# Performance work log

Hardware: AMD Instinct MI355X
Metric: run time of the kernel (lower is better)

Reference implementation:

```python
import jax, jax.numpy as jnp
import numpy as np

B, S, D = 4, 2048, 1024
H = 16
DH = D // H


def setup_inputs() -> dict:
    key = jax.random.key(0)
    ks = jax.random.split(key, 5)
    scale = 1.0 / np.sqrt(D)
    return {
        "x": jax.random.normal(ks[0], (B, S, D), dtype=jnp.float32),
        "wq": jax.random.normal(ks[1], (D, D), dtype=jnp.float32) * scale,
        "wk": jax.random.normal(ks[2], (D, D), dtype=jnp.float32) * scale,
        "wv": jax.random.normal(ks[3], (D, D), dtype=jnp.float32) * scale,
        "wo": jax.random.normal(ks[4], (D, D), dtype=jnp.float32) * scale,
    }


def reference(x, wq, wk, wv, wo):
    b, s, d = x.shape
    # nn.Linear applies x @ W.T (weights are [out, in])
    q = (x @ wq.T).reshape(b, s, H, DH).transpose(0, 2, 1, 3)  # [b,h,s,dh]
    k = (x @ wk.T).reshape(b, s, H, DH).transpose(0, 2, 1, 3)
    v = (x @ wv.T).reshape(b, s, H, DH).transpose(0, 2, 1, 3)
    scale = 1.0 / jnp.sqrt(jnp.asarray(DH, dtype=x.dtype))
    scores = jnp.einsum("bhqd,bhkd->bhqk", q, k) * scale  # [b,h,s,s]
    causal = jnp.tril(jnp.ones((s, s), dtype=bool))
    scores = jnp.where(causal, scores, -jnp.inf)
    attn = jax.nn.softmax(scores, axis=-1)
    out = jnp.einsum("bhqk,bhkd->bhqd", attn, v)  # [b,h,s,dh]
    out = out.transpose(0, 2, 1, 3).reshape(b, s, d)
    return out @ wo.T
```

## Files before the change

kernel.cpp:

```cpp
#include <hip/hip_runtime.h>
#include <hip/hip_bf16.h>

#define Bz 4
#define Sz 2048
#define Dz 1024
#define Hz 16
#define DHz 64

typedef __bf16 bf16x8 __attribute__((ext_vector_type(8)));
typedef float f32x4 __attribute__((ext_vector_type(4)));
typedef short s16x4 __attribute__((ext_vector_type(4)));
typedef unsigned short u16x4 __attribute__((ext_vector_type(4)));

__global__ __launch_bounds__(256) void cvt_f32_bf16(const float* __restrict__ src,
                                                    __hip_bfloat16* __restrict__ dst, int n) {
    int i = (blockIdx.x * 256 + threadIdx.x) * 4;
    if (i >= n) return;
    float4 f = *reinterpret_cast<const float4*>(src + i);
    dst[i + 0] = __float2bfloat16(f.x);
    dst[i + 1] = __float2bfloat16(f.y);
    dst[i + 2] = __float2bfloat16(f.z);
    dst[i + 3] = __float2bfloat16(f.w);
}

__global__ __launch_bounds__(256) void cvt_w4(const float* __restrict__ w0, const float* __restrict__ w1,
                                              const float* __restrict__ w2, const float* __restrict__ w3,
                                              __hip_bfloat16* __restrict__ dst) {
    constexpr int WEL = Dz * Dz;
    int i = (blockIdx.x * 256 + threadIdx.x) * 4;
    const int which = i >> 20;
    const float* src = (which == 0) ? w0 : (which == 1) ? w1 : (which == 2) ? w2 : w3;
    float4 f = *reinterpret_cast<const float4*>(src + (i & (WEL - 1)));
    dst[i + 0] = __float2bfloat16(f.x);
    dst[i + 1] = __float2bfloat16(f.y);
    dst[i + 2] = __float2bfloat16(f.z);
    dst[i + 3] = __float2bfloat16(f.w);
}

__device__ __forceinline__ void gl2lds16(const __hip_bfloat16* g, __hip_bfloat16* l) {
    __builtin_amdgcn_global_load_lds(
        (const __attribute__((address_space(1))) void*)g,
        (__attribute__((address_space(3))) void*)l, 16, 0, 0);
}

__device__ __forceinline__ unsigned ldsaddr(const void* p) {
    return (unsigned)(size_t)(const __attribute__((address_space(3))) void*)p;
}

template <int N, int K, typename OT, int MODE>
__device__ __forceinline__ void gemm128_body(const __hip_bfloat16* __restrict__ A,
                                             const __hip_bfloat16* __restrict__ W,
                                             OT* __restrict__ C, int bm, int bn,
                                             __hip_bfloat16* As, __hip_bfloat16* Bs) {
    const int tid  = threadIdx.x;
    const int wid  = tid >> 6;
    const int lane = tid & 63;
    const int quad = lane >> 4;
    const int l16  = lane & 15;
    const int wr = wid >> 1, wc = wid & 1;

    const int srow = wid * 32 + (lane >> 2);
    const int scol = (lane & 3) * 8;
    const __hip_bfloat16* gA = A + (size_t)(bm * 128 + srow) * K + scol;
    const __hip_bfloat16* gB = W + (size_t)(bn * 128 + srow) * K + scol;
    __hip_bfloat16* lA = &As[(wid * 32) * 32];
    __hip_bfloat16* lB = &Bs[(wid * 32) * 32];

    f32x4 acc[4][4] = {};

    for (int k0 = 0; k0 < K; k0 += 32) {
        __syncthreads();
        gl2lds16(gA + k0,                  lA);
        gl2lds16(gA + (size_t)16 * K + k0, lA + 16 * 32);
        gl2lds16(gB + k0,                  lB);
        gl2lds16(gB + (size_t)16 * K + k0, lB + 16 * 32);
        __syncthreads();

        bf16x8 af[4], bf[4];
#pragma unroll
        for (int mi = 0; mi < 4; ++mi)
            af[mi] = *reinterpret_cast<const bf16x8*>(&As[(wr * 64 + mi * 16 + l16) * 32 + quad * 8]);
#pragma unroll
        for (int ni = 0; ni < 4; ++ni)
            bf[ni] = *reinterpret_cast<const bf16x8*>(&Bs[(wc * 64 + ni * 16 + l16) * 32 + quad * 8]);
#pragma unroll
        for (int mi = 0; mi < 4; ++mi)
#pragma unroll
            for (int ni = 0; ni < 4; ++ni)
                acc[mi][ni] = __builtin_amdgcn_mfma_f32_16x16x32_bf16(af[mi], bf[ni], acc[mi][ni], 0, 0, 0);
    }

#pragma unroll
    for (int mi = 0; mi < 4; ++mi)
#pragma unroll
        for (int ni = 0; ni < 4; ++ni) {
            const int row0 = bm * 128 + wr * 64 + mi * 16 + quad * 4;
            const int col  = bn * 128 + wc * 64 + ni * 16 + l16;
#pragma unroll
            for (int r = 0; r < 4; ++r) {
                const int row = row0 + r;
                if constexpr (MODE == 0) {
                    if constexpr (__is_same(OT, float))
                        C[(size_t)row * N + col] = acc[mi][ni][r];
                    else
                        C[(size_t)row * N + col] = __float2bfloat16(acc[mi][ni][r]);
                } else if constexpr (MODE == 1) {
                    const int bh = (row >> 11) * Hz + (col >> 6);
                    C[(size_t)bh * (Sz * DHz) + (size_t)(row & 2047) * 64 + (col & 63)] =
                        __float2bfloat16(acc[mi][ni][r]);
                } else {
                    const int bh = (row >> 11) * Hz + (col >> 6);
                    C[(size_t)bh * (Sz * DHz) + (size_t)((col >> 4) & 3) * (Sz * 16) +
                      (size_t)(row & 2047) * 16 + (col & 15)] = __float2bfloat16(acc[mi][ni][r]);
                }
            }
        }
}

template <int M, int N, int K, typename OT>
__global__ __launch_bounds__(256) void gemm128(const __hip_bfloat16* __restrict__ A,
                                               const __hip_bfloat16* __restrict__ W,
                                               OT* __restrict__ C) {
    __shared__ __hip_bfloat16 As[128 * 32];
    __shared__ __hip_bfloat16 Bs[128 * 32];
    constexpr int NB = N / 128;
    gemm128_body<N, K, OT, 0>(A, W, C, blockIdx.x / NB, blockIdx.x % NB, As, Bs);
}

template <int M, int K>
__global__ __launch_bounds__(256) void gemm_qkv(const __hip_bfloat16* __restrict__ A,
                                                const __hip_bfloat16* __restrict__ W0,
                                                const __hip_bfloat16* __restrict__ W1,
                                                const __hip_bfloat16* __restrict__ W2,
                                                __hip_bfloat16* __restrict__ C0,
                                                __hip_bfloat16* __restrict__ C1,
                                                __hip_bfloat16* __restrict__ C2) {
    __shared__ __hip_bfloat16 As[128 * 32];
    __shared__ __hip_bfloat16 Bs[128 * 32];
    constexpr int NB = Dz / 128;
    const int which = blockIdx.x % 3;
    const int rem   = blockIdx.x / 3;
    const int bm = rem / NB, bn = rem % NB;
    if (which == 0)      gemm128_body<Dz, K, __hip_bfloat16, 0>(A, W0, C0, bm, bn, As, Bs);
    else if (which == 1) gemm128_body<Dz, K, __hip_bfloat16, 1>(A, W1, C1, bm, bn, As, Bs);
    else                 gemm128_body<Dz, K, __hip_bfloat16, 2>(A, W2, C2, bm, bn, As, Bs);
}

__device__ __forceinline__ f32x4 mfma16bf(s16x4 a, s16x4 b, f32x4 c) {
#if __has_builtin(__builtin_amdgcn_mfma_f32_16x16x16bf16_1k)
    return __builtin_amdgcn_mfma_f32_16x16x16bf16_1k(a, b, c, 0, 0, 0);
#else
    asm volatile("v_mfma_f32_16x16x16_bf16 %0, %1, %2, %0" : "+v"(c) : "v"(a), "v"(b));
    return c;
#endif
}

#define TRD(i, off) \
    asm volatile("ds_read_b64_tr_b16 %0, %1 offset:" off : "=v"(vf[i]) : "v"(va))

__global__ __launch_bounds__(256, 4) void attn_mfma6(const __hip_bfloat16* __restrict__ Q,
                                                     const __hip_bfloat16* __restrict__ Kh,
                                                     const __hip_bfloat16* __restrict__ Vh,
                                                     __hip_bfloat16* __restrict__ O) {
    __shared__ __hip_bfloat16 Ks[2][64 * 64];
    __shared__ __hip_bfloat16 Vs[2][64 * 64];

    const int tid  = threadIdx.x;
    const int wid  = tid >> 6;
    const int lane = tid & 63;
    const int quad = lane >> 4;
    const int l16  = lane & 15;

    const int xcd  = blockIdx.x & 7;
    const int j    = blockIdx.x >> 3;
    const int bh   = xcd * 8 + (j >> 4);
    const int pair = j & 15;
    const int h    = bh & 15;
    const int b    = bh >> 4;
    const size_t baseQ = (size_t)b * Sz * Dz + (size_t)h * DHz;
    const size_t kvb   = (size_t)bh * (Sz * DHz);

    const int rlo = lane >> 3;
    const int xel = ((lane & 7) ^ rlo) * 8;

    auto stage = [&](int kn, int bf_) {
#pragma unroll
        for (int c = 0; c < 2; ++c) {
            gl2lds16(Kh + kvb + (size_t)(kn + wid * 16 + c * 8 + rlo) * 64 + xel,
                     &Ks[bf_][(wid * 16 + c * 8) * 64]);
            gl2lds16(Vh + kvb + (size_t)wid * (Sz * 16) + (size_t)(kn + c * 32 + (lane >> 1)) * 16 + (lane & 1) * 8,
                     &Vs[bf_][wid * 1024 + c * 512]);
        }
    };

    const unsigned vb0 = ldsaddr(&Vs[0][0]) + lane * 8;
    const unsigned sw  = (l16 & 7) << 4;

    constexpr float SC = 0.18033688011112042f;

    int buf = 0;
    stage(0, 0);
    __syncthreads();

#pragma unroll 1
    for (int p = 0; p < 2; ++p) {
        const int qblk  = (p == 0) ? pair : 31 - pair;
        const int q0    = qblk * 64 + wid * 16;
        const int niter = qblk + 1;

        const __hip_bfloat16* qp = Q + baseQ + (size_t)(q0 + l16) * Dz + quad * 8;
        const bf16x8 qf0 = *reinterpret_cast<const bf16x8*>(qp);
        const bf16x8 qf1 = *reinterpret_cast<const bf16x8*>(qp + 32);

        float m = -1e30f, l = 0.f;
        f32x4 ot[4] = {};

#pragma unroll 1
        for (int it = 0; it < niter; ++it) {
            const int k0 = it * 64;

            f32x4 st[4] = {};
            {
                const char* Kp = (const char*)&Ks[buf][0];
#pragma unroll
                for (int s = 0; s < 4; ++s) {
                    const int rb = (s * 16 + l16) * 128;
                    const bf16x8 a0 = *reinterpret_cast<const bf16x8*>(Kp + rb + ((quad * 16) ^ sw));
                    const bf16x8 a1 = *reinterpret_cast<const bf16x8*>(Kp + rb + ((quad * 16 + 64) ^ sw));
                    st[s] = __builtin_amdgcn_mfma_f32_16x16x32_bf16(a0, qf0, st[s], 0, 0, 0);
                    st[s] = __builtin_amdgcn_mfma_f32_16x16x32_bf16(a1, qf1, st[s], 0, 0, 0);
                }
            }

            const bool more = (it + 1 < niter);
            if (more)        stage(k0 + 64, buf ^ 1);
            else if (p == 0) stage(0,       buf ^ 1);

            float sv[16];
            if (it == niter - 1) {
                const int qrow = q0 + l16;
#pragma unroll
                for (int s = 0; s < 4; ++s)
#pragma unroll
                    for (int r = 0; r < 4; ++r) {
                        const int key = k0 + s * 16 + quad * 4 + r;
                        sv[s * 4 + r] = (key <= qrow) ? st[s][r] * SC : -1e30f;
                    }
            } else {
#pragma unroll
                for (int s = 0; s < 4; ++s)
#pragma unroll
                    for (int r = 0; r < 4; ++r) sv[s * 4 + r] = st[s][r] * SC;
            }

            float mx[8];
#pragma unroll
            for (int i = 0; i < 8; ++i) mx[i] = fmaxf(sv[2 * i], sv[2 * i + 1]);
#pragma unroll
            for (int i = 0; i < 4; ++i) mx[i] = fmaxf(mx[2 * i], mx[2 * i + 1]);
            float tmax = fmaxf(fmaxf(mx[0], mx[1]), fmaxf(mx[2], mx[3]));
            tmax = fmaxf(tmax, __shfl_xor(tmax, 16, 64));
            tmax = fmaxf(tmax, __shfl_xor(tmax, 32, 64));

            const float mnew = fmaxf(m, tmax);
            const bool  skip = __all(tmax <= m);
            float alpha = 1.f;
            if (!skip) { alpha = __builtin_amdgcn_exp2f(m - mnew); m = mnew; }

            float pv[16];
#pragma unroll
            for (int i = 0; i < 16; ++i) pv[i] = __builtin_amdgcn_exp2f(sv[i] - m);

            float ad[8];
#pragma unroll
            for (int i = 0; i < 8; ++i) ad[i] = pv[2 * i] + pv[2 * i + 1];
#pragma unroll
            for (int i = 0; i < 4; ++i) ad[i] = ad[2 * i] + ad[2 * i + 1];
            float psum = (ad[0] + ad[1]) + (ad[2] + ad[3]);
            psum += __shfl_xor(psum, 16, 64);
            psum += __shfl_xor(psum, 32, 64);
            l = l * alpha + psum;

            s16x4 vf[16];
            const unsigned va = vb0 + (unsigned)(buf << 13);
            TRD(0, "0");    TRD(1, "512");  TRD(2, "1024"); TRD(3, "1536");
            TRD(4, "2048"); TRD(5, "2560"); TRD(6, "3072"); TRD(7, "3584");

            s16x4 pw[4];
#pragma unroll
            for (int s = 0; s < 4; ++s)
#pragma unroll
                for (int r = 0; r < 4; ++r) {
                    union { __hip_bfloat16 hh; short uu; } cv;
                    cv.hh = __float2bfloat16(pv[s * 4 + r]);
                    pw[s][r] = cv.uu;
                }
            if (!skip) {
#pragma unroll
                for (int s = 0; s < 4; ++s) ot[s] *= alpha;
            }

            asm volatile("s_waitcnt lgkmcnt(0)" ::: "memory");
            __builtin_amdgcn_sched_barrier(0);
            TRD(8,  "4096"); TRD(9,  "4608"); TRD(10, "5120"); TRD(11, "5632");
            TRD(12, "6144"); TRD(13, "6656"); TRD(14, "7168"); TRD(15, "7680");

            ot[0] = mfma16bf(vf[0],  pw[0], ot[0]);
            ot[0] = mfma16bf(vf[1],  pw[1], ot[0]);
            ot[0] = mfma16bf(vf[2],  pw[2], ot[0]);
            ot[0] = mfma16bf(vf[3],  pw[3], ot[0]);
            ot[1] = mfma16bf(vf[4],  pw[0], ot[1]);
            ot[1] = mfma16bf(vf[5],  pw[1], ot[1]);
            ot[1] = mfma16bf(vf[6],  pw[2], ot[1]);
            ot[1] = mfma16bf(vf[7],  pw[3], ot[1]);

            asm volatile("s_waitcnt lgkmcnt(0)" ::: "memory");
            __builtin_amdgcn_sched_barrier(0);
            ot[2] = mfma16bf(vf[8],  pw[0], ot[2]);
            ot[2] = mfma16bf(vf[9],  pw[1], ot[2]);
            ot[2] = mfma16bf(vf[10], pw[2], ot[2]);
            ot[2] = mfma16bf(vf[11], pw[3], ot[2]);
            ot[3] = mfma16bf(vf[12], pw[0], ot[3]);
            ot[3] = mfma16bf(vf[13], pw[1], ot[3]);
            ot[3] = mfma16bf(vf[14], pw[2], ot[3]);
            ot[3] = mfma16bf(vf[15], pw[3], ot[3]);

            __syncthreads();
            buf ^= 1;
        }

        const float linv = 1.f / l;
        __hip_bfloat16* op = O + baseQ + (size_t)(q0 + l16) * Dz + quad * 4;
#pragma unroll
        for (int sd = 0; sd < 4; ++sd) {
            u16x4 w;
#pragma unroll
            for (int r = 0; r < 4; ++r) {
                union { __hip_bfloat16 hh; unsigned short uu; } cv;
                cv.hh = __float2bfloat16(ot[sd][r] * linv);
                w[r] = cv.uu;
            }
            *reinterpret_cast<u16x4*>(op + sd * 16) = w;
        }
    }
}

extern "C" void kernel_launch(void* const* d_in, const int* in_sizes, int n_in,
                              void* d_out, int out_size, void* d_ws, size_t ws_size,
                              hipStream_t stream) {
    const float* x  = (const float*)d_in[0];
    const float* wq = (const float*)d_in[1];
    const float* wk = (const float*)d_in[2];
    const float* wv = (const float*)d_in[3];
    const float* wo = (const float*)d_in[4];
    float* out = (float*)d_out;

    constexpr int TOK = Bz * Sz * Dz;
    constexpr int WEL = Dz * Dz;

    __hip_bfloat16* xb  = (__hip_bfloat16*)d_ws;
    __hip_bfloat16* wqb = xb  + TOK;
    __hip_bfloat16* wkb = wqb + WEL;
    __hip_bfloat16* wvb = wkb + WEL;
    __hip_bfloat16* wob = wvb + WEL;
    __hip_bfloat16* Qb  = wob + WEL;
    __hip_bfloat16* Kh  = Qb + TOK;
    __hip_bfloat16* Vh  = (__hip_bfloat16*)d_out;
    __hip_bfloat16* Ob  = xb;

    cvt_f32_bf16<<<TOK / 4 / 256, 256, 0, stream>>>(x, xb, TOK);
    cvt_w4<<<4 * WEL / 4 / 256, 256, 0, stream>>>(wq, wk, wv, wo, wqb);

    constexpr int M = Bz * Sz;
    constexpr int GB = (M / 128) * (Dz / 128);

    gemm_qkv<M, Dz><<<3 * GB, 256, 0, stream>>>(xb, wqb, wkb, wvb, Qb, Kh, Vh);

    const int ATTN_BLOCKS = Bz * Hz * 16;
    attn_mfma6<<<ATTN_BLOCKS, 256, 0, stream>>>(Qb, Kh, Vh, Ob);

    gemm128<M, Dz, Dz, float><<<GB, 256, 0, stream>>>(Ob, wob, out);
}
```

Measured before the change: 249.5 us.

## Fold softmax scale into Q projection and compute row sums with MFMA

Multiplies the softmax scale (with log2e) into Q in the QKV GEMM epilogue, so the attention kernel no longer scales every score. The per-row probability sum is now accumulated by MFMA against a vector of ones instead of a VALU add tree plus cross-lane shuffles. The running max uses a flatter fmax chain, and alpha rescaling moves inside the non-skip branch. This trades VALU and shuffle work for a few extra MFMAs per tile, and rounding Q to bf16 after scaling slightly changes numerics.

```diff
diff --git a/kernel.cpp b/kernel.cpp
--- a/kernel.cpp
+++ b/kernel.cpp
@@ -11,6 +11,8 @@
 typedef float f32x4 __attribute__((ext_vector_type(4)));
 typedef short s16x4 __attribute__((ext_vector_type(4)));
 typedef unsigned short u16x4 __attribute__((ext_vector_type(4)));
+
+#define SCQF 0.18033688011112042f
 
 __global__ __launch_bounds__(256) void cvt_f32_bf16(const float* __restrict__ src,
                                                     __hip_bfloat16* __restrict__ dst, int n) {
@@ -47,7 +49,7 @@
     return (unsigned)(size_t)(const __attribute__((address_space(3))) void*)p;
 }
 
-template <int N, int K, typename OT, int MODE>
+template <int N, int K, typename OT, int MODE, bool SCQ = false>
 __device__ __forceinline__ void gemm128_body(const __hip_bfloat16* __restrict__ A,
                                              const __hip_bfloat16* __restrict__ W,
                                              OT* __restrict__ C, int bm, int bn,
@@ -99,19 +101,21 @@
 #pragma unroll
             for (int r = 0; r < 4; ++r) {
                 const int row = row0 + r;
+                float v = acc[mi][ni][r];
+                if constexpr (SCQ) v *= SCQF;
                 if constexpr (MODE == 0) {
                     if constexpr (__is_same(OT, float))
-                        C[(size_t)row * N + col] = acc[mi][ni][r];
+                        C[(size_t)row * N + col] = v;
                     else
-                        C[(size_t)row * N + col] = __float2bfloat16(acc[mi][ni][r]);
+                        C[(size_t)row * N + col] = __float2bfloat16(v);
                 } else if constexpr (MODE == 1) {
                     const int bh = (row >> 11) * Hz + (col >> 6);
                     C[(size_t)bh * (Sz * DHz) + (size_t)(row & 2047) * 64 + (col & 63)] =
-                        __float2bfloat16(acc[mi][ni][r]);
+                        __float2bfloat16(v);
                 } else {
                     const int bh = (row >> 11) * Hz + (col >> 6);
                     C[(size_t)bh * (Sz * DHz) + (size_t)((col >> 4) & 3) * (Sz * 16) +
-                      (size_t)(row & 2047) * 16 + (col & 15)] = __float2bfloat16(acc[mi][ni][r]);
+                      (size_t)(row & 2047) * 16 + (col & 15)] = __float2bfloat16(v);
                 }
             }
         }
@@ -141,7 +145,7 @@
     const int which = blockIdx.x % 3;
     const int rem   = blockIdx.x / 3;
     const int bm = rem / NB, bn = rem % NB;
-    if (which == 0)      gemm128_body<Dz, K, __hip_bfloat16, 0>(A, W0, C0, bm, bn, As, Bs);
+    if (which == 0)      gemm128_body<Dz, K, __hip_bfloat16, 0, true>(A, W0, C0, bm, bn, As, Bs);
     else if (which == 1) gemm128_body<Dz, K, __hip_bfloat16, 1>(A, W1, C1, bm, bn, As, Bs);
     else                 gemm128_body<Dz, K, __hip_bfloat16, 2>(A, W2, C2, bm, bn, As, Bs);
 }
@@ -158,7 +162,7 @@
 #define TRD(i, off) \
     asm volatile("ds_read_b64_tr_b16 %0, %1 offset:" off : "=v"(vf[i]) : "v"(va))
 
-__global__ __launch_bounds__(256, 4) void attn_mfma6(const __hip_bfloat16* __restrict__ Q,
+__global__ __launch_bounds__(256, 4) void attn_mfma7(const __hip_bfloat16* __restrict__ Q,
                                                      const __hip_bfloat16* __restrict__ Kh,
                                                      const __hip_bfloat16* __restrict__ Vh,
                                                      __hip_bfloat16* __restrict__ O) {
@@ -196,7 +200,7 @@
     const unsigned vb0 = ldsaddr(&Vs[0][0]) + lane * 8;
     const unsigned sw  = (l16 & 7) << 4;
 
-    constexpr float SC = 0.18033688011112042f;
+    const s16x4 ones = {(short)0x3F80, (short)0x3F80, (short)0x3F80, (short)0x3F80};
 
     int buf = 0;
     stage(0, 0);
@@ -212,8 +216,9 @@
         const bf16x8 qf0 = *reinterpret_cast<const bf16x8*>(qp);
         const bf16x8 qf1 = *reinterpret_cast<const bf16x8*>(qp + 32);
 
-        float m = -1e30f, l = 0.f;
+        float m = -1e30f;
         f32x4 ot[4] = {};
+        f32x4 lacc  = {};
 
 #pragma unroll 1
         for (int it = 0; it < niter; ++it) {
@@ -244,42 +249,38 @@
 #pragma unroll
                     for (int r = 0; r < 4; ++r) {
                         const int key = k0 + s * 16 + quad * 4 + r;
-                        sv[s * 4 + r] = (key <= qrow) ? st[s][r] * SC : -1e30f;
+                        sv[s * 4 + r] = (key <= qrow) ? st[s][r] : -1e30f;
                     }
             } else {
 #pragma unroll
                 for (int s = 0; s < 4; ++s)
 #pragma unroll
-                    for (int r = 0; r < 4; ++r) sv[s * 4 + r] = st[s][r] * SC;
-            }
-
-            float mx[8];
-#pragma unroll
-            for (int i = 0; i < 8; ++i) mx[i] = fmaxf(sv[2 * i], sv[2 * i + 1]);
-#pragma unroll
-            for (int i = 0; i < 4; ++i) mx[i] = fmaxf(mx[2 * i], mx[2 * i + 1]);
-            float tmax = fmaxf(fmaxf(mx[0], mx[1]), fmaxf(mx[2], mx[3]));
+                    for (int r = 0; r < 4; ++r) sv[s * 4 + r] = st[s][r];
+            }
+
+            const float p0 = fmaxf(fmaxf(sv[0],  sv[1]),  sv[2]);
+            const float p1 = fmaxf(fmaxf(sv[3],  sv[4]),  sv[5]);
+            const float p2 = fmaxf(fmaxf(sv[6],  sv[7]),  sv[8]);
+            const float p3 = fmaxf(fmaxf(sv[9],  sv[10]), sv[11]);
+            const float p4 = fmaxf(fmaxf(sv[12], sv[13]), sv[14]);
+            const float p5 = fmaxf(fmaxf(p0, p1), p2);
+            float tmax = fmaxf(fmaxf(fmaxf(p5, p3), p4), sv[15]);
             tmax = fmaxf(tmax, __shfl_xor(tmax, 16, 64));
             tmax = fmaxf(tmax, __shfl_xor(tmax, 32, 64));
 
             const float mnew = fmaxf(m, tmax);
             const bool  skip = __all(tmax <= m);
-            float alpha = 1.f;
-            if (!skip) { alpha = __builtin_amdgcn_exp2f(m - mnew); m = mnew; }
+            if (!skip) {
+                const float alpha = __builtin_amdgcn_exp2f(m - mnew);
+                m = mnew;
+#pragma unroll
+                for (int s = 0; s < 4; ++s) ot[s] *= alpha;
+                lacc[0] *= alpha;
+            }
 
             float pv[16];
 #pragma unroll
             for (int i = 0; i < 16; ++i) pv[i] = __builtin_amdgcn_exp2f(sv[i] - m);
-
-            float ad[8];
-#pragma unroll
-            for (int i = 0; i < 8; ++i) ad[i] = pv[2 * i] + pv[2 * i + 1];
-#pragma unroll
-            for (int i = 0; i < 4; ++i) ad[i] = ad[2 * i] + ad[2 * i + 1];
-            float psum = (ad[0] + ad[1]) + (ad[2] + ad[3]);
-            psum += __shfl_xor(psum, 16, 64);
-            psum += __shfl_xor(psum, 32, 64);
-            l = l * alpha + psum;
 
             s16x4 vf[16];
             const unsigned va = vb0 + (unsigned)(buf << 13);
@@ -295,10 +296,11 @@
                     cv.hh = __float2bfloat16(pv[s * 4 + r]);
                     pw[s][r] = cv.uu;
                 }
-            if (!skip) {
-#pragma unroll
-                for (int s = 0; s < 4; ++s) ot[s] *= alpha;
-            }
+
+            lacc = mfma16bf(ones, pw[0], lacc);
+            lacc = mfma16bf(ones, pw[1], lacc);
+            lacc = mfma16bf(ones, pw[2], lacc);
+            lacc = mfma16bf(ones, pw[3], lacc);
 
             asm volatile("s_waitcnt lgkmcnt(0)" ::: "memory");
             __builtin_amdgcn_sched_barrier(0);
@@ -329,7 +331,7 @@
             buf ^= 1;
         }
 
-        const float linv = 1.f / l;
+        const float linv = 1.f / lacc[0];
         __hip_bfloat16* op = O + baseQ + (size_t)(q0 + l16) * Dz + quad * 4;
 #pragma unroll
         for (int sd = 0; sd < 4; ++sd) {
@@ -377,7 +379,7 @@
     gemm_qkv<M, Dz><<<3 * GB, 256, 0, stream>>>(xb, wqb, wkb, wvb, Qb, Kh, Vh);
 
     const int ATTN_BLOCKS = Bz * Hz * 16;
-    attn_mfma6<<<ATTN_BLOCKS, 256, 0, stream>>>(Qb, Kh, Vh, Ob);
+    attn_mfma7<<<ATTN_BLOCKS, 256, 0, stream>>>(Qb, Kh, Vh, Ob);
 
     gemm128<M, Dz, Dz, float><<<GB, 256, 0, stream>>>(Ob, wob, out);
 }
```

Measured after the change: 247.4 us. No clear change (-0.8%).
